# Optimization experiments

Measured on AMD Instinct MI355X. Metric: run time of the kernel, lower is better.

Reference implementation:

```python
import jax, jax.numpy as jnp
import numpy as np

B, N, E, D = 32, 144, 127, 512   # batch, seq (forced to 144 by additive PE), embed_size, encoding_size
H, DK, DV = 8, 64, 64            # heads, dim_k, dim_v
F = 32 * D                       # forward_expansion=32 (default)
L = 4                            # num_layers
EPS = 1e-5


def setup_inputs() -> dict:
    key = jax.random.key(0)
    ks = jax.random.split(key, 20)
    s = 0.02
    x = jax.random.normal(ks[0], (B, N, E), jnp.float32)
    # causal mask: True = masked (future positions)
    future_mask = jnp.broadcast_to(jnp.triu(jnp.ones((N, N), bool), k=1), (B, N, N))
    inp = {
        'batch_size': B,
        'x': x,
        'future_mask': future_mask,
        'Wenc': jax.random.normal(ks[1], (E + 1, D), jnp.float32) * s,
        'benc': jnp.zeros((D,), jnp.float32),
        'Wq': jax.random.normal(ks[2], (L, D, H * DK), jnp.float32) * s,
        'Wk': jax.random.normal(ks[3], (L, D, H * DK), jnp.float32) * s,
        'Wv': jax.random.normal(ks[4], (L, D, H * DV), jnp.float32) * s,
        'Wo': jax.random.normal(ks[5], (L, H * DV, D), jnp.float32) * s,
        'bo': jnp.zeros((L, D), jnp.float32),
        'ln1_g': jnp.ones((L, D), jnp.float32), 'ln1_b': jnp.zeros((L, D), jnp.float32),
        'ln2_g': jnp.ones((L, D), jnp.float32), 'ln2_b': jnp.zeros((L, D), jnp.float32),
        'ln3_g': jnp.ones((L, D), jnp.float32), 'ln3_b': jnp.zeros((L, D), jnp.float32),
        'W1': jax.random.normal(ks[6], (L, D, F), jnp.float32) * s,
        'b1': jnp.zeros((L, F), jnp.float32),
        'W2': jax.random.normal(ks[7], (L, F, D), jnp.float32) * s,
        'b2': jnp.zeros((L, D), jnp.float32),
        'Wdec': jax.random.normal(ks[8], (D, E), jnp.float32) * s,
        'bdec': jnp.zeros((E,), jnp.float32),
    }
    return inp


def _layernorm(x, g, b):
    mu = jnp.mean(x, axis=-1, keepdims=True)
    var = jnp.var(x, axis=-1, keepdims=True)
    return (x - mu) * jax.lax.rsqrt(var + EPS) * g + b


def _mha(values_in, keys_in, query_in, mask, Wq, Wk, Wv, Wo, bo):
    b = query_in.shape[0]
    q = (query_in @ Wq).reshape(b, -1, H, DK).transpose(0, 2, 1, 3)   # [b,H,N,DK]
    k = (keys_in @ Wk).reshape(b, -1, H, DK).transpose(0, 2, 1, 3)
    v = (values_in @ Wv).reshape(b, -1, H, DV).transpose(0, 2, 1, 3)  # [b,H,N,DV]
    scores = jnp.einsum('bhnk,bhmk->bhnm', q, k)  # NOTE: no 1/sqrt(dk) scaling in original
    if mask is not None:
        scores = jnp.where(mask[:, None, :, :], jnp.float32(-1e20), scores)
    attn = jax.nn.softmax(scores, axis=-1)
    # torch.einsum('bhnn,bhnv->bhnv') takes the DIAGONAL of attn and scales v elementwise
    diag = jnp.diagonal(attn, axis1=2, axis2=3)  # [b,H,N]
    out = diag[..., None] * v                    # [b,H,N,DV]
    out = out.transpose(0, 2, 1, 3).reshape(b, -1, H * DV)
    return out @ Wo + bo


def reference(batch_size, x, future_mask, Wenc, benc, Wq, Wk, Wv, Wo, bo,
              ln1_g, ln1_b, ln2_g, ln2_b, ln3_g, ln3_b, W1, b1, W2, b2, Wdec, bdec):
    # Additive positional encoding: append arange(N)/max as extra channel
    pe = (jnp.arange(N, dtype=jnp.float32) / jnp.float32(N - 1))[None, :, None]
    xp = jnp.concatenate([x, jnp.broadcast_to(pe, (x.shape[0], N, 1))], axis=2)
    xe = xp @ Wenc + benc  # [B,N,D]
    out = xe
    for l in range(L):
        a = _mha(out, out, out, future_mask, Wq[l], Wk[l], Wv[l], Wo[l], bo[l])
        q = _layernorm(a + xe, ln1_g[l], ln1_b[l])
        a = _mha(xe, xe, q, None, Wq[l], Wk[l], Wv[l], Wo[l], bo[l])
        ff = jax.nn.relu(a @ W1[l] + b1[l]) @ W2[l] + b2[l]
        ao = _layernorm(ff + a, ln2_g[l], ln2_b[l])
        ff2 = jax.nn.relu(ao @ W1[l] + b1[l]) @ W2[l] + b2[l]
        out = _layernorm(ao + ff2, ln3_g[l], ln3_b[l])
    return out @ Wdec + bdec  # [B,N,E]
```

## Files before the change

### kernel.cpp

```cpp
#include <hip/hip_runtime.h>
#include <stdint.h>


typedef unsigned short u16;
typedef unsigned int   u32;
typedef __attribute__((ext_vector_type(8))) short s16x8;
typedef __attribute__((ext_vector_type(4))) float f32x4;

#define AS1 __attribute__((address_space(1)))
#define AS3 __attribute__((address_space(3)))

__device__ __forceinline__ float bf2f(u16 h) { return __uint_as_float(((u32)h) << 16); }
__device__ __forceinline__ u16 f2bf(float f) {
  u32 u = __float_as_uint(f);
  u32 r = (u + 0x7fffu + ((u >> 16) & 1u)) >> 16;
  return (u16)r;
}
__device__ __forceinline__ void gl_lds16(const u16* g, u16* l) {
  __builtin_amdgcn_global_load_lds((const AS1 void*)g, (AS3 void*)l, 16, 0, 0);
}

template<bool BIAS, bool RELU, bool OBF, bool XCD>
__global__ __launch_bounds__(512, 2)
void gemm256(const u16* __restrict__ A, int lda,
             const u16* __restrict__ Bt, int ldb,
             void* __restrict__ Cv, int ldc,
             const float* __restrict__ bias,
             int K, long long sstride, int mtiles)
{
  __shared__ __align__(16) u16 L[3][2][256 * 32];
  const int tid  = threadIdx.x;
  const int wave = tid >> 6, lane = tid & 63;

  int bid = blockIdx.x;
  if (XCD) {
    const int cpx = gridDim.x >> 3;
    bid = (bid & 7) * cpx + (bid >> 3);
  }
  const int mt = bid % mtiles, nt = bid / mtiles;
  const int m0 = mt * 256, n0 = nt * 256;
  const long long koff = (long long)blockIdx.z * K;
  A  += (size_t)m0 * lda + koff;
  Bt += (size_t)n0 * ldb + koff;

  const int row0 = tid >> 2;
  const int kq_s = (tid & 3) ^ ((row0 >> 1) & 3);
  const size_t offA0 = (size_t)row0 * lda + kq_s * 8;
  const size_t offA1 = offA0 + (size_t)128 * lda;
  const size_t offB0 = (size_t)row0 * ldb + kq_s * 8;
  const size_t offB1 = offB0 + (size_t)128 * ldb;

  const int wr = (wave >> 2) * 128, wc = (wave & 3) * 64;
  const int fr = lane & 15, kqe = lane >> 4;
  const int skq = kqe ^ ((fr >> 1) & 3);

  f32x4 acc[8][4] = {};
  const int NT = K >> 5;

  {
    const u16* Ak = A;            const u16* Bk = Bt;
    gl_lds16(Ak + offA0, &L[0][0][tid * 8]);
    gl_lds16(Ak + offA1, &L[0][0][tid * 8 + 4096]);
    gl_lds16(Bk + offB0, &L[0][1][tid * 8]);
    gl_lds16(Bk + offB1, &L[0][1][tid * 8 + 4096]);
    Ak += 32; Bk += 32;
    gl_lds16(Ak + offA0, &L[1][0][tid * 8]);
    gl_lds16(Ak + offA1, &L[1][0][tid * 8 + 4096]);
    gl_lds16(Bk + offB0, &L[1][1][tid * 8]);
    gl_lds16(Bk + offB1, &L[1][1][tid * 8 + 4096]);
  }

  int cur = 0, pre = 2;
  for (int t = 0; t < NT; ++t) {
    if (t + 1 < NT) asm volatile("s_waitcnt vmcnt(4)" ::: "memory");
    else            asm volatile("s_waitcnt vmcnt(0)" ::: "memory");
    __builtin_amdgcn_s_barrier();
    __builtin_amdgcn_sched_barrier(0);

    if (t + 2 < NT) {
      const u16* Ak = A + (size_t)(t + 2) * 32;
      const u16* Bk = Bt + (size_t)(t + 2) * 32;
      u16* sA = &L[pre][0][0];
      u16* sB = &L[pre][1][0];
      gl_lds16(Ak + offA0, sA + tid * 8);
      gl_lds16(Ak + offA1, sA + tid * 8 + 4096);
      gl_lds16(Bk + offB0, sB + tid * 8);
      gl_lds16(Bk + offB1, sB + tid * 8 + 4096);
    }

    const u16* Ab = &L[cur][0][0];
    const u16* Bb = &L[cur][1][0];
    s16x8 af[8], bf[4];
#pragma unroll
    for (int i = 0; i < 8; ++i)
      af[i] = *(const s16x8*)&Ab[((wr + i * 16 + fr) * 4 + skq) * 8];
#pragma unroll
    for (int j = 0; j < 4; ++j)
      bf[j] = *(const s16x8*)&Bb[((wc + j * 16 + fr) * 4 + skq) * 8];

    __builtin_amdgcn_s_setprio(1);
#pragma unroll
    for (int i = 0; i < 8; ++i)
#pragma unroll
      for (int j = 0; j < 4; ++j)
        acc[i][j] = __builtin_amdgcn_mfma_f32_16x16x32_bf16(af[i], bf[j], acc[i][j], 0, 0, 0);
    __builtin_amdgcn_s_setprio(0);
    __builtin_amdgcn_sched_barrier(0);

    cur = (cur == 2) ? 0 : cur + 1;
    pre = (pre == 2) ? 0 : pre + 1;
  }

#pragma unroll
  for (int j = 0; j < 4; ++j) {
    const int ccol = n0 + wc + j * 16 + fr;
    const float bv = BIAS ? bias[ccol] : 0.0f;
#pragma unroll
    for (int i = 0; i < 8; ++i) {
#pragma unroll
      for (int r = 0; r < 4; ++r) {
        const int crow = m0 + wr + i * 16 + kqe * 4 + r;
        float v = acc[i][j][r] + bv;
        if (RELU) v = fmaxf(v, 0.0f);
        if (OBF) ((u16*)Cv)[(size_t)crow * ldc + ccol] = f2bf(v);
        else ((float*)Cv + (size_t)blockIdx.z * sstride)[(size_t)crow * ldc + ccol] = v;
      }
    }
  }
}

template<bool BIAS, bool RELU, bool OBF>
__global__ __launch_bounds__(256, 2)
void gemm_bt(const u16* __restrict__ A, int lda,
             const u16* __restrict__ Bt, int ldb,
             void* __restrict__ Cv, int ldc,
             const float* __restrict__ bias,
             int K, int nreal, long long sstride)
{
  __shared__ __align__(16) u16 As[2][128 * 64];
  __shared__ __align__(16) u16 Bs[2][128 * 64];
  const int tid  = threadIdx.x;
  const int wave = tid >> 6, lane = tid & 63;
  const int m0 = blockIdx.x * 128, n0 = blockIdx.y * 128;
  const long long koff = (long long)blockIdx.z * K;
  A  += (size_t)m0 * lda + koff;
  Bt += (size_t)n0 * ldb + koff;

  const int r0 = tid >> 3;
  const int sp = ((tid & 7) ^ (r0 & 7)) * 8;
  const u16* gA = A  + (size_t)r0 * lda + sp;
  const u16* gB = Bt + (size_t)r0 * ldb + sp;
  u16* lA = &As[0][tid * 8];
  u16* lB = &Bs[0][tid * 8];

  const int wr = (wave >> 1) * 64, wc = (wave & 1) * 64;
  const int fr = lane & 15, kq = lane >> 4;
  const int s0 = ((0 * 4 + kq) ^ (fr & 7)) * 8;
  const int s1 = ((1 * 4 + kq) ^ (fr & 7)) * 8;

  f32x4 acc[4][4] = {};
  const int NT = K >> 6;

#pragma unroll
  for (int q = 0; q < 4; ++q) gl_lds16(gA + (size_t)q * 32 * lda, lA + q * 2048);
#pragma unroll
  for (int q = 0; q < 4; ++q) gl_lds16(gB + (size_t)q * 32 * ldb, lB + q * 2048);
  gA += 64; gB += 64;

  for (int t = 0; t < NT; ++t) {
    __syncthreads();
    const int cur = t & 1;
    if (t + 1 < NT) {
      u16* dA = lA + (cur ^ 1) * (128 * 64);
      u16* dB = lB + (cur ^ 1) * (128 * 64);
#pragma unroll
      for (int q = 0; q < 4; ++q) gl_lds16(gA + (size_t)q * 32 * lda, dA + q * 2048);
#pragma unroll
      for (int q = 0; q < 4; ++q) gl_lds16(gB + (size_t)q * 32 * ldb, dB + q * 2048);
      gA += 64; gB += 64;
    }
    const u16* Ab = &As[cur][0];
    const u16* Bb = &Bs[cur][0];
    s16x8 a0[4], a1[4], b0[4], b1[4];
#pragma unroll
    for (int i = 0; i < 4; ++i) {
      const int ra = (wr + i * 16 + fr) * 64;
      a0[i] = *(const s16x8*)&Ab[ra + s0];
      a1[i] = *(const s16x8*)&Ab[ra + s1];
    }
#pragma unroll
    for (int j = 0; j < 4; ++j) {
      const int rb = (wc + j * 16 + fr) * 64;
      b0[j] = *(const s16x8*)&Bb[rb + s0];
      b1[j] = *(const s16x8*)&Bb[rb + s1];
    }
#pragma unroll
    for (int i = 0; i < 4; ++i)
#pragma unroll
      for (int j = 0; j < 4; ++j)
        acc[i][j] = __builtin_amdgcn_mfma_f32_16x16x32_bf16(a0[i], b0[j], acc[i][j], 0, 0, 0);
#pragma unroll
    for (int i = 0; i < 4; ++i)
#pragma unroll
      for (int j = 0; j < 4; ++j)
        acc[i][j] = __builtin_amdgcn_mfma_f32_16x16x32_bf16(a1[i], b1[j], acc[i][j], 0, 0, 0);
  }

#pragma unroll
  for (int j = 0; j < 4; ++j) {
    const int ccol = n0 + wc + j * 16 + fr;
    if (ccol >= nreal) continue;
    const float bv = BIAS ? bias[ccol] : 0.0f;
#pragma unroll
    for (int i = 0; i < 4; ++i) {
#pragma unroll
      for (int r = 0; r < 4; ++r) {
        const int crow = m0 + wr + i * 16 + kq * 4 + r;
        float v = acc[i][j][r] + bv;
        if (RELU) v = fmaxf(v, 0.0f);
        if (OBF) ((u16*)Cv)[(size_t)crow * ldc + ccol] = f2bf(v);
        else ((float*)Cv + (size_t)blockIdx.z * sstride)[(size_t)crow * ldc + ccol] = v;
      }
    }
  }
}

__global__ void tcvt(u16* __restrict__ Wt, const float* __restrict__ W,
                     int K, int N, int Npad)
{
  __shared__ float t[32][33];
  const int n0 = blockIdx.x * 32, k0 = blockIdx.y * 32;
  const int tx = threadIdx.x, ty = threadIdx.y;
#pragma unroll
  for (int i = 0; i < 4; ++i) {
    int k = k0 + ty + i * 8, n = n0 + tx;
    t[ty + i * 8][tx] = (k < K && n < N) ? W[(size_t)k * N + n] : 0.f;
  }
  __syncthreads();
#pragma unroll
  for (int i = 0; i < 4; ++i) {
    int n = n0 + ty + i * 8, k = k0 + tx;
    if (n < Npad) Wt[(size_t)n * K + k] = f2bf(t[tx][ty + i * 8]);
  }
}

template<bool CAUSAL>
__global__ __launch_bounds__(192)
void attn_diag(float* __restrict__ diag,
               const u16* __restrict__ Q, int ldq,
               const u16* __restrict__ Kp, int ldk)
{
  __shared__ float Kl[144][64];
  const int bh = blockIdx.x;
  const int b = bh >> 3, h = bh & 7;
  const int tid = threadIdx.x;

  for (int c = tid; c < 144 * 8; c += 192) {
    int m = c >> 3, c8 = c & 7;
    uint4 u = *(const uint4*)(Kp + (size_t)(b * 144 + m) * ldk + h * 64 + c8 * 8);
    float* dst = &Kl[m][c8 * 8];
    dst[0] = __uint_as_float(u.x << 16); dst[1] = __uint_as_float(u.x & 0xffff0000u);
    dst[2] = __uint_as_float(u.y << 16); dst[3] = __uint_as_float(u.y & 0xffff0000u);
    dst[4] = __uint_as_float(u.z << 16); dst[5] = __uint_as_float(u.z & 0xffff0000u);
    dst[6] = __uint_as_float(u.w << 16); dst[7] = __uint_as_float(u.w & 0xffff0000u);
  }
  __syncthreads();
  if (tid >= 144) return;
  const int n = tid;
  float q[64];
  const uint4* qp = (const uint4*)(Q + (size_t)(b * 144 + n) * ldq + h * 64);
#pragma unroll
  for (int c = 0; c < 8; ++c) {
    uint4 u = qp[c];
    q[c*8+0] = __uint_as_float(u.x << 16); q[c*8+1] = __uint_as_float(u.x & 0xffff0000u);
    q[c*8+2] = __uint_as_float(u.y << 16); q[c*8+3] = __uint_as_float(u.y & 0xffff0000u);
    q[c*8+4] = __uint_as_float(u.z << 16); q[c*8+5] = __uint_as_float(u.z & 0xffff0000u);
    q[c*8+6] = __uint_as_float(u.w << 16); q[c*8+7] = __uint_as_float(u.w & 0xffff0000u);
  }
  const int mmax = CAUSAL ? n : 143;
  float mx = -3.4e38f, sm = 0.f, sdiag = 0.f;
  for (int m = 0; m <= mmax; ++m) {
    float s0 = 0, s1 = 0, s2 = 0, s3 = 0;
#pragma unroll
    for (int c = 0; c < 64; c += 4) {
      s0 = fmaf(q[c + 0], Kl[m][c + 0], s0);
      s1 = fmaf(q[c + 1], Kl[m][c + 1], s1);
      s2 = fmaf(q[c + 2], Kl[m][c + 2], s2);
      s3 = fmaf(q[c + 3], Kl[m][c + 3], s3);
    }
    float s = (s0 + s1) + (s2 + s3);
    if (m == n) sdiag = s;
    float nmx = fmaxf(mx, s);
    sm = sm * __expf(mx - nmx) + __expf(s - nmx);
    mx = nmx;
  }
  diag[(size_t)bh * 144 + n] = __expf(sdiag - mx) / sm;
}

__global__ void scale_v(u16* __restrict__ outb, const float* __restrict__ diag,
                        const u16* __restrict__ V, int ldv)
{
  const int idx = blockIdx.x * 256 + threadIdx.x;
  const int r = idx >> 9, d = idx & 511;
  const int b = r / 144, n = r - b * 144;
  const int h = d >> 6;
  const float dg = diag[((size_t)b * 8 + h) * 144 + n];
  outb[(size_t)r * 512 + d] = f2bf(dg * bf2f(V[(size_t)r * ldv + d]));
}

__global__ __launch_bounds__(128)
void ln_dual(float* __restrict__ outf, u16* __restrict__ outb,
             const float* __restrict__ A, const float* __restrict__ Bv,
             const float* __restrict__ g, const float* __restrict__ be)
{
  const int r = blockIdx.x, t = threadIdx.x;
  float4 a = ((const float4*)(A + (size_t)r * 512))[t];
  float4 b = ((const float4*)(Bv + (size_t)r * 512))[t];
  const float x0 = a.x + b.x, x1 = a.y + b.y, x2 = a.z + b.z, x3 = a.w + b.w;
  float s = x0 + x1 + x2 + x3;
  float q = x0 * x0 + x1 * x1 + x2 * x2 + x3 * x3;
#pragma unroll
  for (int off = 32; off > 0; off >>= 1) { s += __shfl_down(s, off); q += __shfl_down(q, off); }
  __shared__ float ss[2], qs[2];
  if ((t & 63) == 0) { ss[t >> 6] = s; qs[t >> 6] = q; }
  __syncthreads();
  s = ss[0] + ss[1]; q = qs[0] + qs[1];
  const float mean = s * (1.f / 512.f);
  const float var  = q * (1.f / 512.f) - mean * mean;
  const float rs = rsqrtf(var + 1e-5f);
  float4 gg = ((const float4*)g)[t];
  float4 bb = ((const float4*)be)[t];
  const float o0 = (x0 - mean) * rs * gg.x + bb.x;
  const float o1 = (x1 - mean) * rs * gg.y + bb.y;
  const float o2 = (x2 - mean) * rs * gg.z + bb.z;
  const float o3 = (x3 - mean) * rs * gg.w + bb.w;
  if (outf) ((float4*)(outf + (size_t)r * 512))[t] = make_float4(o0, o1, o2, o3);
  if (outb) {
    uint2 u;
    u.x = (u32)f2bf(o0) | ((u32)f2bf(o1) << 16);
    u.y = (u32)f2bf(o2) | ((u32)f2bf(o3) << 16);
    ((uint2*)(outb + (size_t)r * 512))[t] = u;
  }
}

__global__ void f32_to_bf16_vec(u16* __restrict__ o, const float* __restrict__ a)
{
  const int i = blockIdx.x * 256 + threadIdx.x;
  float4 v = ((const float4*)a)[i];
  uint2 u;
  u.x = (u32)f2bf(v.x) | ((u32)f2bf(v.y) << 16);
  u.y = (u32)f2bf(v.z) | ((u32)f2bf(v.w) << 16);
  ((uint2*)o)[i] = u;
}

__global__ void reduce_ff(float* __restrict__ ff, const float* __restrict__ parts,
                          const float* __restrict__ bias)
{
  const int i = blockIdx.x * 256 + threadIdx.x;
  float4 acc = ((const float4*)bias)[i & 127];
#pragma unroll
  for (int s = 0; s < 8; ++s) {
    float4 p = ((const float4*)(parts + (size_t)s * 4608 * 512))[i];
    acc.x += p.x; acc.y += p.y; acc.z += p.z; acc.w += p.w;
  }
  ((float4*)ff)[i] = acc;
}

__global__ void build_xp(u16* __restrict__ xp, const float* __restrict__ x)
{
  const int i = blockIdx.x * 256 + threadIdx.x;
  const int r = i >> 7, e = i & 127;
  const float v = (e < 127) ? x[(size_t)r * 127 + e] : (float)(r % 144) * (1.f / 143.f);
  xp[i] = f2bf(v);
}

extern "C" void kernel_launch(void* const* d_in, const int* in_sizes, int n_in,
                              void* d_out, int out_size, void* d_ws, size_t ws_size,
                              hipStream_t stream)
{
  (void)in_sizes; (void)n_in; (void)out_size; (void)ws_size;
  const float* x    = (const float*)d_in[1];
  const float* Wenc = (const float*)d_in[3];
  const float* benc = (const float*)d_in[4];
  const float* Wq   = (const float*)d_in[5];
  const float* Wk   = (const float*)d_in[6];
  const float* Wv   = (const float*)d_in[7];
  const float* Wo   = (const float*)d_in[8];
  const float* bo   = (const float*)d_in[9];
  const float* ln1g = (const float*)d_in[10];
  const float* ln1b = (const float*)d_in[11];
  const float* ln2g = (const float*)d_in[12];
  const float* ln2b = (const float*)d_in[13];
  const float* ln3g = (const float*)d_in[14];
  const float* ln3b = (const float*)d_in[15];
  const float* W1   = (const float*)d_in[16];
  const float* b1   = (const float*)d_in[17];
  const float* W2   = (const float*)d_in[18];
  const float* b2   = (const float*)d_in[19];
  const float* Wdec = (const float*)d_in[20];
  const float* bdec = (const float*)d_in[21];

  char* w = (char*)d_ws;
  auto alloc = [&](size_t bytes) { void* p = (void*)w; w += (bytes + 255) & ~(size_t)255; return p; };
  u16*   wt_qkv = (u16*)alloc((size_t)1536 * 512 * 2);
  u16*   wt_o   = (u16*)alloc((size_t)512 * 512 * 2);
  u16*   wt_1   = (u16*)alloc((size_t)16384 * 512 * 2);
  u16*   wt_2   = (u16*)alloc((size_t)512 * 16384 * 2);
  u16*   wt_enc = (u16*)alloc((size_t)512 * 128 * 2);
  u16*   wt_dec = (u16*)alloc((size_t)128 * 512 * 2);
  float* xe_f   = (float*)alloc((size_t)4608 * 512 * 4);
  u16*   xe_bf  = (u16*)alloc((size_t)4608 * 512 * 2);
  u16*   out_bf = (u16*)alloc((size_t)4608 * 512 * 2);
  u16*   qkv_bf = (u16*)alloc((size_t)4608 * 1536 * 2);
  float* diag   = (float*)alloc((size_t)256 * 144 * 4);
  u16*   attn_bf= (u16*)alloc((size_t)4608 * 512 * 2);
  float* a1     = (float*)alloc((size_t)4608 * 512 * 4);
  u16*   qln_bf = (u16*)alloc((size_t)4608 * 512 * 2);
  float* a2     = (float*)alloc((size_t)4608 * 512 * 4);
  u16*   a2_bf  = (u16*)alloc((size_t)4608 * 512 * 2);
  u16*   hidden = (u16*)alloc((size_t)4608 * 16384 * 2);
  float* parts  = (float*)alloc((size_t)8 * 4608 * 512 * 4);
  float* ff     = (float*)alloc((size_t)4608 * 512 * 4);
  float* ao_f   = (float*)alloc((size_t)4608 * 512 * 4);
  u16*   ao_bf  = (u16*)alloc((size_t)4608 * 512 * 2);
  float* ff2    = a1;
  u16*   xp_bf  = hidden;

  const long long PSTRIDE = (long long)4608 * 512;

  tcvt<<<dim3(16, 4), dim3(32, 8), 0, stream>>>(wt_enc, Wenc, 128, 512, 512);
  tcvt<<<dim3(4, 16), dim3(32, 8), 0, stream>>>(wt_dec, Wdec, 512, 127, 128);
  build_xp<<<2304, 256, 0, stream>>>(xp_bf, x);
  gemm_bt<true, false, false><<<dim3(36, 4, 1), 256, 0, stream>>>(
      xp_bf, 128, wt_enc, 128, xe_f, 512, benc, 128, 512, 0);
  f32_to_bf16_vec<<<2304, 256, 0, stream>>>(xe_bf, xe_f);

  const u16* in_bf = xe_bf;
  for (int l = 0; l < 4; ++l) {
    const size_t wsz = (size_t)512 * 512;
    tcvt<<<dim3(16, 16), dim3(32, 8), 0, stream>>>(wt_qkv,               Wq + l * wsz, 512, 512, 512);
    tcvt<<<dim3(16, 16), dim3(32, 8), 0, stream>>>(wt_qkv + 512 * 512,   Wk + l * wsz, 512, 512, 512);
    tcvt<<<dim3(16, 16), dim3(32, 8), 0, stream>>>(wt_qkv + 1024 * 512,  Wv + l * wsz, 512, 512, 512);
    tcvt<<<dim3(16, 16), dim3(32, 8), 0, stream>>>(wt_o, Wo + l * wsz, 512, 512, 512);
    tcvt<<<dim3(512, 16), dim3(32, 8), 0, stream>>>(wt_1, W1 + (size_t)l * 512 * 16384, 512, 16384, 16384);
    tcvt<<<dim3(16, 512), dim3(32, 8), 0, stream>>>(wt_2, W2 + (size_t)l * 16384 * 512, 16384, 512, 512);

    gemm_bt<false, false, true><<<dim3(36, 12, 1), 256, 0, stream>>>(
        in_bf, 512, wt_qkv, 512, qkv_bf, 1536, nullptr, 512, 1536, 0);
    attn_diag<true><<<256, 192, 0, stream>>>(diag, qkv_bf, 1536, qkv_bf + 512, 1536);
    scale_v<<<9216, 256, 0, stream>>>(attn_bf, diag, qkv_bf + 1024, 1536);
    gemm_bt<true, false, false><<<dim3(36, 4, 1), 256, 0, stream>>>(
        attn_bf, 512, wt_o, 512, a1, 512, bo + l * 512, 512, 512, 0);
    ln_dual<<<4608, 128, 0, stream>>>(nullptr, qln_bf, a1, xe_f, ln1g + l * 512, ln1b + l * 512);

    gemm_bt<false, false, true><<<dim3(36, 4, 1), 256, 0, stream>>>(
        qln_bf, 512, wt_qkv, 512, attn_bf, 512, nullptr, 512, 512, 0);
    gemm_bt<false, false, true><<<dim3(36, 8, 1), 256, 0, stream>>>(
        xe_bf, 512, wt_qkv + 512 * 512, 512, qkv_bf, 1024, nullptr, 512, 1024, 0);
    attn_diag<false><<<256, 192, 0, stream>>>(diag, attn_bf, 512, qkv_bf, 1024);
    scale_v<<<9216, 256, 0, stream>>>(attn_bf, diag, qkv_bf + 512, 1024);
    gemm_bt<true, false, false><<<dim3(36, 4, 1), 256, 0, stream>>>(
        attn_bf, 512, wt_o, 512, a2, 512, bo + l * 512, 512, 512, 0);
    f32_to_bf16_vec<<<2304, 256, 0, stream>>>(a2_bf, a2);

    gemm256<true, true, true, true><<<dim3(1152, 1, 1), 512, 0, stream>>>(
        a2_bf, 512, wt_1, 512, hidden, 16384, b1 + l * 16384, 512, 0, 18);
    gemm256<false, false, false, false><<<dim3(36, 1, 8), 512, 0, stream>>>(
        hidden, 16384, wt_2, 16384, parts, 512, nullptr, 2048, PSTRIDE, 18);
    reduce_ff<<<2304, 256, 0, stream>>>(ff, parts, b2 + l * 512);
    ln_dual<<<4608, 128, 0, stream>>>(ao_f, ao_bf, ff, a2, ln2g + l * 512, ln2b + l * 512);

    gemm256<true, true, true, true><<<dim3(1152, 1, 1), 512, 0, stream>>>(
        ao_bf, 512, wt_1, 512, hidden, 16384, b1 + l * 16384, 512, 0, 18);
    gemm256<false, false, false, false><<<dim3(36, 1, 8), 512, 0, stream>>>(
        hidden, 16384, wt_2, 16384, parts, 512, nullptr, 2048, PSTRIDE, 18);
    reduce_ff<<<2304, 256, 0, stream>>>(ff2, parts, b2 + l * 512);
    ln_dual<<<4608, 128, 0, stream>>>(nullptr, out_bf, ao_f, ff2, ln3g + l * 512, ln3b + l * 512);
    in_bf = out_bf;
  }

  gemm_bt<true, false, false><<<dim3(36, 1, 1), 256, 0, stream>>>(
      in_bf, 512, wt_dec, 512, (float*)d_out, 127, bdec, 512, 127, 0);
}
```

Baseline: 3.530 ms.

## Rework FFN GEMM pipeline to BK=64 double-buffer and fuse reduce/convert kernels

The large FFN GEMM switches from a three-stage, 32-wide K pipeline to a two-buffer, 64-wide K pipeline. The next tile's loads are split across the two MFMA half-steps, with an XOR swizzle over 8 chunks. All layer weights are converted in batched launches up front, not per layer. The split-K partial reduce is fused into the layernorm kernel, and the bf16 copy of the attention output is written directly from the GEMM epilogue. The aim is fewer launches and less memory traffic, but the full vmcnt(0) wait per stage may expose load latency in the dominant GEMMs.

Result: slower. 10.45 ms (+196.1%).

```diff
diff --git a/kernel.cpp b/kernel.cpp
--- a/kernel.cpp
+++ b/kernel.cpp
@@ -28,7 +28,7 @@
              const float* __restrict__ bias,
              int K, long long sstride, int mtiles)
 {
-  __shared__ __align__(16) u16 L[3][2][256 * 32];
+  __shared__ __align__(16) u16 L[2][2][256 * 64];
   const int tid  = threadIdx.x;
   const int wave = tid >> 6, lane = tid & 63;
 
@@ -43,72 +43,82 @@
   A  += (size_t)m0 * lda + koff;
   Bt += (size_t)n0 * ldb + koff;
 
-  const int row0 = tid >> 2;
-  const int kq_s = (tid & 3) ^ ((row0 >> 1) & 3);
-  const size_t offA0 = (size_t)row0 * lda + kq_s * 8;
-  const size_t offA1 = offA0 + (size_t)128 * lda;
-  const size_t offB0 = (size_t)row0 * ldb + kq_s * 8;
-  const size_t offB1 = offB0 + (size_t)128 * ldb;
-
+  int srow[4], scol[4];
+#pragma unroll
+  for (int q = 0; q < 4; ++q) {
+    const int ci = tid + q * 512;
+    srow[q] = ci >> 3;
+    scol[q] = ((ci & 7) ^ (srow[q] & 7)) * 8;
+  }
+  auto STAGE_A = [&](int buf, int t) {
+#pragma unroll
+    for (int q = 0; q < 4; ++q)
+      gl_lds16(A + (size_t)t * 64 + (size_t)srow[q] * lda + scol[q],
+               &L[buf][0][(tid + q * 512) * 8]);
+  };
+  auto STAGE_B = [&](int buf, int t) {
+#pragma unroll
+    for (int q = 0; q < 4; ++q)
+      gl_lds16(Bt + (size_t)t * 64 + (size_t)srow[q] * ldb + scol[q],
+               &L[buf][1][(tid + q * 512) * 8]);
+  };
+
+  const int fr = lane & 15, kq = lane >> 4;
   const int wr = (wave >> 2) * 128, wc = (wave & 3) * 64;
-  const int fr = lane & 15, kqe = lane >> 4;
-  const int skq = kqe ^ ((fr >> 1) & 3);
+
+  auto LDA_ = [&](int buf, int half, s16x8* af) {
+#pragma unroll
+    for (int i = 0; i < 8; ++i) {
+      const int row = wr + i * 16 + fr;
+      af[i] = *(const s16x8*)&L[buf][0][(row * 8 + ((half * 4 + kq) ^ (row & 7))) * 8];
+    }
+  };
+  auto LDB_ = [&](int buf, int half, s16x8* bf) {
+#pragma unroll
+    for (int j = 0; j < 4; ++j) {
+      const int row = wc + j * 16 + fr;
+      bf[j] = *(const s16x8*)&L[buf][1][(row * 8 + ((half * 4 + kq) ^ (row & 7))) * 8];
+    }
+  };
 
   f32x4 acc[8][4] = {};
-  const int NT = K >> 5;
-
-  {
-    const u16* Ak = A;            const u16* Bk = Bt;
-    gl_lds16(Ak + offA0, &L[0][0][tid * 8]);
-    gl_lds16(Ak + offA1, &L[0][0][tid * 8 + 4096]);
-    gl_lds16(Bk + offB0, &L[0][1][tid * 8]);
-    gl_lds16(Bk + offB1, &L[0][1][tid * 8 + 4096]);
-    Ak += 32; Bk += 32;
-    gl_lds16(Ak + offA0, &L[1][0][tid * 8]);
-    gl_lds16(Ak + offA1, &L[1][0][tid * 8 + 4096]);
-    gl_lds16(Bk + offB0, &L[1][1][tid * 8]);
-    gl_lds16(Bk + offB1, &L[1][1][tid * 8 + 4096]);
-  }
-
-  int cur = 0, pre = 2;
-  for (int t = 0; t < NT; ++t) {
-    if (t + 1 < NT) asm volatile("s_waitcnt vmcnt(4)" ::: "memory");
-    else            asm volatile("s_waitcnt vmcnt(0)" ::: "memory");
+  auto MM = [&](s16x8* a, s16x8* b) {
+    __builtin_amdgcn_s_setprio(1);
+#pragma unroll
+    for (int i = 0; i < 8; ++i)
+#pragma unroll
+      for (int j = 0; j < 4; ++j)
+        acc[i][j] = __builtin_amdgcn_mfma_f32_16x16x32_bf16(a[i], b[j], acc[i][j], 0, 0, 0);
+    __builtin_amdgcn_s_setprio(0);
+  };
+
+  const int NT = K >> 6;
+  STAGE_A(0, 0); STAGE_B(0, 0);
+
+  for (int t = 0; t < NT; t += 2) {
+    asm volatile("s_waitcnt vmcnt(0)" ::: "memory");
     __builtin_amdgcn_s_barrier();
-    __builtin_amdgcn_sched_barrier(0);
-
-    if (t + 2 < NT) {
-      const u16* Ak = A + (size_t)(t + 2) * 32;
-      const u16* Bk = Bt + (size_t)(t + 2) * 32;
-      u16* sA = &L[pre][0][0];
-      u16* sB = &L[pre][1][0];
-      gl_lds16(Ak + offA0, sA + tid * 8);
-      gl_lds16(Ak + offA1, sA + tid * 8 + 4096);
-      gl_lds16(Bk + offB0, sB + tid * 8);
-      gl_lds16(Bk + offB1, sB + tid * 8 + 4096);
-    }
-
-    const u16* Ab = &L[cur][0][0];
-    const u16* Bb = &L[cur][1][0];
-    s16x8 af[8], bf[4];
-#pragma unroll
-    for (int i = 0; i < 8; ++i)
-      af[i] = *(const s16x8*)&Ab[((wr + i * 16 + fr) * 4 + skq) * 8];
-#pragma unroll
-    for (int j = 0; j < 4; ++j)
-      bf[j] = *(const s16x8*)&Bb[((wc + j * 16 + fr) * 4 + skq) * 8];
-
-    __builtin_amdgcn_s_setprio(1);
-#pragma unroll
-    for (int i = 0; i < 8; ++i)
-#pragma unroll
-      for (int j = 0; j < 4; ++j)
-        acc[i][j] = __builtin_amdgcn_mfma_f32_16x16x32_bf16(af[i], bf[j], acc[i][j], 0, 0, 0);
-    __builtin_amdgcn_s_setprio(0);
-    __builtin_amdgcn_sched_barrier(0);
-
-    cur = (cur == 2) ? 0 : cur + 1;
-    pre = (pre == 2) ? 0 : pre + 1;
+    {
+      s16x8 a[8], b[4];
+      LDA_(0, 0, a); LDB_(0, 0, b);
+      if (t + 1 < NT) STAGE_A(1, t + 1);
+      MM(a, b);
+      LDA_(0, 1, a); LDB_(0, 1, b);
+      if (t + 1 < NT) STAGE_B(1, t + 1);
+      MM(a, b);
+    }
+    if (t + 1 >= NT) break;
+    asm volatile("s_waitcnt vmcnt(0)" ::: "memory");
+    __builtin_amdgcn_s_barrier();
+    {
+      s16x8 a[8], b[4];
+      LDA_(1, 0, a); LDB_(1, 0, b);
+      if (t + 2 < NT) STAGE_A(0, t + 2);
+      MM(a, b);
+      LDA_(1, 1, a); LDB_(1, 1, b);
+      if (t + 2 < NT) STAGE_B(0, t + 2);
+      MM(a, b);
+    }
   }
 
 #pragma unroll
@@ -119,7 +129,7 @@
     for (int i = 0; i < 8; ++i) {
 #pragma unroll
       for (int r = 0; r < 4; ++r) {
-        const int crow = m0 + wr + i * 16 + kqe * 4 + r;
+        const int crow = m0 + wr + i * 16 + kq * 4 + r;
         float v = acc[i][j][r] + bv;
         if (RELU) v = fmaxf(v, 0.0f);
         if (OBF) ((u16*)Cv)[(size_t)crow * ldc + ccol] = f2bf(v);
@@ -129,11 +139,12 @@
   }
 }
 
-template<bool BIAS, bool RELU, bool OBF>
+template<bool BIAS, bool RELU, bool OBF, bool DUAL>
 __global__ __launch_bounds__(256, 2)
 void gemm_bt(const u16* __restrict__ A, int lda,
              const u16* __restrict__ Bt, int ldb,
              void* __restrict__ Cv, int ldc,
+             u16* __restrict__ C2,
              const float* __restrict__ bias,
              int K, int nreal, long long sstride)
 {
@@ -219,15 +230,21 @@
         float v = acc[i][j][r] + bv;
         if (RELU) v = fmaxf(v, 0.0f);
         if (OBF) ((u16*)Cv)[(size_t)crow * ldc + ccol] = f2bf(v);
-        else ((float*)Cv + (size_t)blockIdx.z * sstride)[(size_t)crow * ldc + ccol] = v;
+        else {
+          ((float*)Cv + (size_t)blockIdx.z * sstride)[(size_t)crow * ldc + ccol] = v;
+          if (DUAL) C2[(size_t)crow * ldc + ccol] = f2bf(v);
+        }
       }
     }
   }
 }
 
-__global__ void tcvt(u16* __restrict__ Wt, const float* __restrict__ W,
-                     int K, int N, int Npad)
-{
+__global__ void tcvt_b(u16* __restrict__ Wt, const float* __restrict__ W,
+                       int K, int N, int Npad,
+                       long long sstride, long long dstride)
+{
+  W  += (size_t)blockIdx.z * sstride;
+  Wt += (size_t)blockIdx.z * dstride;
   __shared__ float t[32][33];
   const int n0 = blockIdx.x * 32, k0 = blockIdx.y * 32;
   const int tx = threadIdx.x, ty = threadIdx.y;
@@ -343,6 +360,48 @@
   }
 }
 
+__global__ __launch_bounds__(128)
+void ln_reduce(float* __restrict__ outf, u16* __restrict__ outb,
+               const float* __restrict__ parts, const float* __restrict__ bias,
+               const float* __restrict__ other,
+               const float* __restrict__ g, const float* __restrict__ be)
+{
+  const long long PS = (long long)4608 * 512;
+  const int r = blockIdx.x, t = threadIdx.x;
+  float4 a = ((const float4*)bias)[t];
+#pragma unroll
+  for (int s = 0; s < 8; ++s) {
+    float4 p = ((const float4*)(parts + (size_t)s * PS + (size_t)r * 512))[t];
+    a.x += p.x; a.y += p.y; a.z += p.z; a.w += p.w;
+  }
+  float4 o = ((const float4*)(other + (size_t)r * 512))[t];
+  const float x0 = a.x + o.x, x1 = a.y + o.y, x2 = a.z + o.z, x3 = a.w + o.w;
+  float s = x0 + x1 + x2 + x3;
+  float q = x0 * x0 + x1 * x1 + x2 * x2 + x3 * x3;
+#pragma unroll
+  for (int off = 32; off > 0; off >>= 1) { s += __shfl_down(s, off); q += __shfl_down(q, off); }
+  __shared__ float ss[2], qs[2];
+  if ((t & 63) == 0) { ss[t >> 6] = s; qs[t >> 6] = q; }
+  __syncthreads();
+  s = ss[0] + ss[1]; q = qs[0] + qs[1];
+  const float mean = s * (1.f / 512.f);
+  const float var  = q * (1.f / 512.f) - mean * mean;
+  const float rs = rsqrtf(var + 1e-5f);
+  float4 gg = ((const float4*)g)[t];
+  float4 bb = ((const float4*)be)[t];
+  const float o0 = (x0 - mean) * rs * gg.x + bb.x;
+  const float o1 = (x1 - mean) * rs * gg.y + bb.y;
+  const float o2 = (x2 - mean) * rs * gg.z + bb.z;
+  const float o3 = (x3 - mean) * rs * gg.w + bb.w;
+  if (outf) ((float4*)(outf + (size_t)r * 512))[t] = make_float4(o0, o1, o2, o3);
+  if (outb) {
+    uint2 u;
+    u.x = (u32)f2bf(o0) | ((u32)f2bf(o1) << 16);
+    u.y = (u32)f2bf(o2) | ((u32)f2bf(o3) << 16);
+    ((uint2*)(outb + (size_t)r * 512))[t] = u;
+  }
+}
+
 __global__ void f32_to_bf16_vec(u16* __restrict__ o, const float* __restrict__ a)
 {
   const int i = blockIdx.x * 256 + threadIdx.x;
@@ -351,19 +410,6 @@
   u.x = (u32)f2bf(v.x) | ((u32)f2bf(v.y) << 16);
   u.y = (u32)f2bf(v.z) | ((u32)f2bf(v.w) << 16);
   ((uint2*)o)[i] = u;
-}
-
-__global__ void reduce_ff(float* __restrict__ ff, const float* __restrict__ parts,
-                          const float* __restrict__ bias)
-{
-  const int i = blockIdx.x * 256 + threadIdx.x;
-  float4 acc = ((const float4*)bias)[i & 127];
-#pragma unroll
-  for (int s = 0; s < 8; ++s) {
-    float4 p = ((const float4*)(parts + (size_t)s * 4608 * 512))[i];
-    acc.x += p.x; acc.y += p.y; acc.z += p.z; acc.w += p.w;
-  }
-  ((float4*)ff)[i] = acc;
 }
 
 __global__ void build_xp(u16* __restrict__ xp, const float* __restrict__ x)
@@ -402,10 +448,10 @@
 
   char* w = (char*)d_ws;
   auto alloc = [&](size_t bytes) { void* p = (void*)w; w += (bytes + 255) & ~(size_t)255; return p; };
-  u16*   wt_qkv = (u16*)alloc((size_t)1536 * 512 * 2);
-  u16*   wt_o   = (u16*)alloc((size_t)512 * 512 * 2);
-  u16*   wt_1   = (u16*)alloc((size_t)16384 * 512 * 2);
-  u16*   wt_2   = (u16*)alloc((size_t)512 * 16384 * 2);
+  u16*   wt_qkv = (u16*)alloc((size_t)4 * 1536 * 512 * 2);
+  u16*   wt_o   = (u16*)alloc((size_t)4 * 512 * 512 * 2);
+  u16*   wt_1   = (u16*)alloc((size_t)4 * 16384 * 512 * 2);
+  u16*   wt_2   = (u16*)alloc((size_t)4 * 512 * 16384 * 2);
   u16*   wt_enc = (u16*)alloc((size_t)512 * 128 * 2);
   u16*   wt_dec = (u16*)alloc((size_t)128 * 512 * 2);
   float* xe_f   = (float*)alloc((size_t)4608 * 512 * 4);
@@ -420,65 +466,68 @@
   u16*   a2_bf  = (u16*)alloc((size_t)4608 * 512 * 2);
   u16*   hidden = (u16*)alloc((size_t)4608 * 16384 * 2);
   float* parts  = (float*)alloc((size_t)8 * 4608 * 512 * 4);
-  float* ff     = (float*)alloc((size_t)4608 * 512 * 4);
   float* ao_f   = (float*)alloc((size_t)4608 * 512 * 4);
   u16*   ao_bf  = (u16*)alloc((size_t)4608 * 512 * 2);
-  float* ff2    = a1;
   u16*   xp_bf  = hidden;
 
   const long long PSTRIDE = (long long)4608 * 512;
-
-  tcvt<<<dim3(16, 4), dim3(32, 8), 0, stream>>>(wt_enc, Wenc, 128, 512, 512);
-  tcvt<<<dim3(4, 16), dim3(32, 8), 0, stream>>>(wt_dec, Wdec, 512, 127, 128);
+  const long long W22 = (long long)512 * 512;
+  const long long WF  = (long long)512 * 16384;
+
+  tcvt_b<<<dim3(16, 4, 1),   dim3(32, 8), 0, stream>>>(wt_enc, Wenc, 128, 512, 512, 0, 0);
+  tcvt_b<<<dim3(4, 16, 1),   dim3(32, 8), 0, stream>>>(wt_dec, Wdec, 512, 127, 128, 0, 0);
+  tcvt_b<<<dim3(16, 16, 4),  dim3(32, 8), 0, stream>>>(wt_qkv,              Wq, 512, 512, 512, W22, (long long)1536 * 512);
+  tcvt_b<<<dim3(16, 16, 4),  dim3(32, 8), 0, stream>>>(wt_qkv + 512 * 512,  Wk, 512, 512, 512, W22, (long long)1536 * 512);
+  tcvt_b<<<dim3(16, 16, 4),  dim3(32, 8), 0, stream>>>(wt_qkv + 1024 * 512, Wv, 512, 512, 512, W22, (long long)1536 * 512);
+  tcvt_b<<<dim3(16, 16, 4),  dim3(32, 8), 0, stream>>>(wt_o, Wo, 512, 512, 512, W22, W22);
+  tcvt_b<<<dim3(512, 16, 4), dim3(32, 8), 0, stream>>>(wt_1, W1, 512, 16384, 16384, WF, WF);
+  tcvt_b<<<dim3(16, 512, 4), dim3(32, 8), 0, stream>>>(wt_2, W2, 16384, 512, 512, WF, WF);
+
   build_xp<<<2304, 256, 0, stream>>>(xp_bf, x);
-  gemm_bt<true, false, false><<<dim3(36, 4, 1), 256, 0, stream>>>(
-      xp_bf, 128, wt_enc, 128, xe_f, 512, benc, 128, 512, 0);
+  gemm_bt<true, false, false, false><<<dim3(36, 4, 1), 256, 0, stream>>>(
+      xp_bf, 128, wt_enc, 128, xe_f, 512, nullptr, benc, 128, 512, 0);
   f32_to_bf16_vec<<<2304, 256, 0, stream>>>(xe_bf, xe_f);
 
   const u16* in_bf = xe_bf;
   for (int l = 0; l < 4; ++l) {
-    const size_t wsz = (size_t)512 * 512;
-    tcvt<<<dim3(16, 16), dim3(32, 8), 0, stream>>>(wt_qkv,               Wq + l * wsz, 512, 512, 512);
-    tcvt<<<dim3(16, 16), dim3(32, 8), 0, stream>>>(wt_qkv + 512 * 512,   Wk + l * wsz, 512, 512, 512);
-    tcvt<<<dim3(16, 16), dim3(32, 8), 0, stream>>>(wt_qkv + 1024 * 512,  Wv + l * wsz, 512, 512, 512);
-    tcvt<<<dim3(16, 16), dim3(32, 8), 0, stream>>>(wt_o, Wo + l * wsz, 512, 512, 512);
-    tcvt<<<dim3(512, 16), dim3(32, 8), 0, stream>>>(wt_1, W1 + (size_t)l * 512 * 16384, 512, 16384, 16384);
-    tcvt<<<dim3(16, 512), dim3(32, 8), 0, stream>>>(wt_2, W2 + (size_t)l * 16384 * 512, 16384, 512, 512);
-
-    gemm_bt<false, false, true><<<dim3(36, 12, 1), 256, 0, stream>>>(
-        in_bf, 512, wt_qkv, 512, qkv_bf, 1536, nullptr, 512, 1536, 0);
+    const u16* wqkv_l = wt_qkv + (size_t)l * 1536 * 512;
+    const u16* wo_l   = wt_o   + (size_t)l * 512 * 512;
+    const u16* w1_l   = wt_1   + (size_t)l * WF;
+    const u16* w2_l   = wt_2   + (size_t)l * WF;
+
+    gemm_bt<false, false, true, false><<<dim3(36, 12, 1), 256, 0, stream>>>(
+        in_bf, 512, wqkv_l, 512, qkv_bf, 1536, nullptr, nullptr, 512, 1536, 0);
     attn_diag<true><<<256, 192, 0, stream>>>(diag, qkv_bf, 1536, qkv_bf + 512, 1536);
     scale_v<<<9216, 256, 0, stream>>>(attn_bf, diag, qkv_bf + 1024, 1536);
-    gemm_bt<true, false, false><<<dim3(36, 4, 1), 256, 0, stream>>>(
-        attn_bf, 512, wt_o, 512, a1, 512, bo + l * 512, 512, 512, 0);
+    gemm_bt<true, false, false, false><<<dim3(36, 4, 1), 256, 0, stream>>>(
+        attn_bf, 512, wo_l, 512, a1, 512, nullptr, bo + l * 512, 512, 512, 0);
     ln_dual<<<4608, 128, 0, stream>>>(nullptr, qln_bf, a1, xe_f, ln1g + l * 512, ln1b + l * 512);
 
-    gemm_bt<false, false, true><<<dim3(36, 4, 1), 256, 0, stream>>>(
-        qln_bf, 512, wt_qkv, 512, attn_bf, 512, nullptr, 512, 512, 0);
-    gemm_bt<false, false, true><<<dim3(36, 8, 1), 256, 0, stream>>>(
-        xe_bf, 512, wt_qkv + 512 * 512, 512, qkv_bf, 1024, nullptr, 512, 1024, 0);
+    gemm_bt<false, false, true, false><<<dim3(36, 4, 1), 256, 0, stream>>>(
+        qln_bf, 512, wqkv_l, 512, attn_bf, 512, nullptr, nullptr, 512, 512, 0);
+    gemm_bt<false, false, true, false><<<dim3(36, 8, 1), 256, 0, stream>>>(
+        xe_bf, 512, wqkv_l + 512 * 512, 512, qkv_bf, 1024, nullptr, nullptr, 512, 1024, 0);
     attn_diag<false><<<256, 192, 0, stream>>>(diag, attn_bf, 512, qkv_bf, 1024);
     scale_v<<<9216, 256, 0, stream>>>(attn_bf, diag, qkv_bf + 512, 1024);
-    gemm_bt<true, false, false><<<dim3(36, 4, 1), 256, 0, stream>>>(
-        attn_bf, 512, wt_o, 512, a2, 512, bo + l * 512, 512, 512, 0);
-    f32_to_bf16_vec<<<2304, 256, 0, stream>>>(a2_bf, a2);
+    gemm_bt<true, false, false, true><<<dim3(36, 4, 1), 256, 0, stream>>>(
+        attn_bf, 512, wo_l, 512, a2, 512, a2_bf, bo + l * 512, 512, 512, 0);
 
     gemm256<true, true, true, true><<<dim3(1152, 1, 1), 512, 0, stream>>>(
-        a2_bf, 512, wt_1, 512, hidden, 16384, b1 + l * 16384, 512, 0, 18);
+        a2_bf, 512, w1_l, 512, hidden, 16384, b1 + l * 16384, 512, 0, 18);
     gemm256<false, false, false, false><<<dim3(36, 1, 8), 512, 0, stream>>>(
-        hidden, 16384, wt_2, 16384, parts, 512, nullptr, 2048, PSTRIDE, 18);
-    reduce_ff<<<2304, 256, 0, stream>>>(ff, parts, b2 + l * 512);
-    ln_dual<<<4608, 128, 0, stream>>>(ao_f, ao_bf, ff, a2, ln2g + l * 512, ln2b + l * 512);
+        hidden, 16384, w2_l, 16384, parts, 512, nullptr, 2048, PSTRIDE, 18);
+    ln_reduce<<<4608, 128, 0, stream>>>(ao_f, ao_bf, parts, b2 + l * 512, a2,
+                                        ln2g + l * 512, ln2b + l * 512);
 
     gemm256<true, true, true, true><<<dim3(1152, 1, 1), 512, 0, stream>>>(
-        ao_bf, 512, wt_1, 512, hidden, 16384, b1 + l * 16384, 512, 0, 18);
+        ao_bf, 512, w1_l, 512, hidden, 16384, b1 + l * 16384, 512, 0, 18);
     gemm256<false, false, false, false><<<dim3(36, 1, 8), 512, 0, stream>>>(
-        hidden, 16384, wt_2, 16384, parts, 512, nullptr, 2048, PSTRIDE, 18);
-    reduce_ff<<<2304, 256, 0, stream>>>(ff2, parts, b2 + l * 512);
-    ln_dual<<<4608, 128, 0, stream>>>(nullptr, out_bf, ao_f, ff2, ln3g + l * 512, ln3b + l * 512);
+        hidden, 16384, w2_l, 16384, parts, 512, nullptr, 2048, PSTRIDE, 18);
+    ln_reduce<<<4608, 128, 0, stream>>>(nullptr, out_bf, parts, b2 + l * 512, ao_f,
+                                        ln3g + l * 512, ln3b + l * 512);
     in_bf = out_bf;
   }
 
-  gemm_bt<true, false, false><<<dim3(36, 1, 1), 256, 0, stream>>>(
-      in_bf, 512, wt_dec, 512, (float*)d_out, 127, bdec, 512, 127, 0);
-}
+  gemm_bt<true, false, false, false><<<dim3(36, 1, 1), 256, 0, stream>>>(
+      in_bf, 512, wt_dec, 512, (float*)d_out, 127, nullptr, bdec, 512, 127, 0);
+}
```
